# Kernel optimization log

Hardware: AMD Instinct MI355X
Metric: run time of the kernel (lower is better)

## Reference

```python
import jax, jax.numpy as jnp
import numpy as np

Z, Y, X = 16, 128, 128
B = 2
N_R, N_L = 12000, 20000   # active voxels per batch element (radar / lidar)
C = 64
IN_DIM = 4
NUM_LAYER = 2
K_LIST = (64, 32)         # knn fan-out = 64 / 2**layer
EPS = 1e-5


def _make_voxels(rng, n_per_batch):
    # unique voxel coords per batch, sorted by linear index (batch-major rows)
    out = []
    for b in range(B):
        lin = np.sort(rng.choice(Z * Y * X, size=n_per_batch, replace=False))
        z = lin // (Y * X); y = (lin // X) % Y; x = lin % X
        out.append(np.stack([np.full(n_per_batch, b), z, y, x], 1))
    return np.concatenate(out, 0).astype(np.int32)


def _nbr_map(coords):
    # 3x3x3 submanifold-conv rulebook: row index of each neighbor, -1 if absent
    b = coords[:, 0].astype(np.int64); z = coords[:, 1]; y = coords[:, 2]; x = coords[:, 3]
    keys = ((b * Z + z) * Y + y) * X + x  # globally sorted
    N = coords.shape[0]
    nbr = np.full((N, 27), -1, np.int64)
    k = 0
    for dz in (-1, 0, 1):
        for dy in (-1, 0, 1):
            for dx in (-1, 0, 1):
                nz, ny, nx = z + dz, y + dy, x + dx
                ok = (nz >= 0) & (nz < Z) & (ny >= 0) & (ny < Y) & (nx >= 0) & (nx < X)
                cand = ((b * Z + nz) * Y + ny) * X + nx
                pos = np.searchsorted(keys, cand)
                pos_c = np.clip(pos, 0, N - 1)
                hit = ok & (keys[pos_c] == cand)
                nbr[:, k] = np.where(hit, pos_c, -1)
                k += 1
    return nbr


def setup_inputs() -> dict:
    rng = np.random.default_rng(0)
    key = jax.random.key(0)
    ks = jax.random.split(key, 16)
    coordsR = _make_voxels(rng, N_R)
    coordsL = _make_voxels(rng, N_L)
    nbrR = _nbr_map(coordsR)
    nbrL = _nbr_map(coordsL)
    NLt = B * N_L
    # knn indices (global row ids into radar rows of same batch)
    knn0 = coordsL[:, 0:1].astype(np.int64) * N_R + rng.integers(0, N_R, (NLt, K_LIST[0]))
    knn1 = coordsL[:, 0:1].astype(np.int64) * N_R + rng.integers(0, N_R, (NLt, K_LIST[1]))
    sc = 1.0 / np.sqrt(27 * C).astype(np.float32)
    inp = {
        "featR": jax.random.normal(ks[0], (B * N_R, IN_DIM), jnp.float32),
        "featL": jax.random.normal(ks[1], (NLt, IN_DIM), jnp.float32),
        "img": jax.random.normal(ks[2], (B, 512), jnp.float32),
        "Win": jax.random.normal(ks[3], (2, IN_DIM, C), jnp.float32) * 0.1,
        "bin_": jnp.zeros((2, C), jnp.float32),
        # [layer, branch(R/L), conv(sp,subm_a,subm_b), 27, Cin, Cout]
        "Wconv": jax.random.normal(ks[4], (NUM_LAYER, 2, 3, 27, C, C), jnp.float32) * sc,
        "bconv": jnp.zeros((NUM_LAYER, 2, 3, C), jnp.float32),
        "bng": jnp.ones((NUM_LAYER, 2, 3, C), jnp.float32),
        "bnb": jnp.zeros((NUM_LAYER, 2, 3, C), jnp.float32),
        "Wimg": jax.random.normal(ks[5], (NUM_LAYER, 512, C), jnp.float32) * 0.05,
        "bimg": jnp.zeros((NUM_LAYER, C), jnp.float32),
        "Wval": jax.random.normal(ks[6], (NUM_LAYER, C, C), jnp.float32) * 0.125,
        "bval": jnp.zeros((NUM_LAYER, C), jnp.float32),
        "Wgate": jax.random.normal(ks[7], (NUM_LAYER, 2 * C, C), jnp.float32) * 0.09,
        "bgate": jnp.zeros((NUM_LAYER, C), jnp.float32),
        "Wbev": jax.random.normal(ks[8], (NUM_LAYER, 2, C * Z, C, 3, 3), jnp.float32) * (1.0 / np.sqrt(C * Z * 9).astype(np.float32)),
        "bbev": jnp.zeros((NUM_LAYER, 2, C), jnp.float32),
        "bntg": jnp.ones((NUM_LAYER, 2, C), jnp.float32),
        "bntb": jnp.zeros((NUM_LAYER, 2, C), jnp.float32),
        "nbrR": jnp.asarray(nbrR),
        "nbrL": jnp.asarray(nbrL),
        "knn0": jnp.asarray(knn0),
        "knn1": jnp.asarray(knn1),
        "coordsR": jnp.asarray(coordsR),
        "coordsL": jnp.asarray(coordsL),
    }
    return inp


def _bn1d(f, g, b):
    m = f.mean(0)
    v = f.var(0)
    return (f - m) / jnp.sqrt(v + EPS) * g + b


def _sconv(f, nbr, W, bias):
    # gather-scatter sparse 3D conv: out[n] = sum_k W[k] @ f[nbr[n,k]]
    mask = (nbr >= 0)[..., None].astype(f.dtype)
    g = f[jnp.clip(nbr, 0)] * mask                 # [N, 27, C]
    return jnp.einsum('nkc,kcd->nd', g, W) + bias


def _branch_block(f, nbr, Wc, bc, g, bt):
    # spconv -> bn -> relu, subm_a -> bn -> relu, subm_b -> bn -> relu
    for j in range(3):
        f = jax.nn.relu(_bn1d(_sconv(f, nbr, Wc[j], bc[j]), g[j], bt[j]))
    return f


def _to_bev(f, coords, Wt, bt, gg, gb):
    dense = jnp.zeros((B, Z, Y, X, C), f.dtype).at[
        coords[:, 0], coords[:, 1], coords[:, 2], coords[:, 3]].add(f)
    x2 = dense.transpose(0, 4, 1, 2, 3).reshape(B, C * Z, Y, X)  # 'b c z y x -> b (c z) y x'
    # ConvTranspose2d(k=3, s=1, p=1) == conv with swapped-IO, spatially flipped kernel, pad 1
    Wk = jnp.transpose(Wt, (1, 0, 2, 3))[:, :, ::-1, ::-1]
    out = jax.lax.conv_general_dilated(x2, Wk, (1, 1), ((1, 1), (1, 1)),
                                       dimension_numbers=('NCHW', 'OIHW', 'NCHW'))
    out = out + bt[:, None, None]
    m = out.mean((0, 2, 3), keepdims=True)
    v = out.var((0, 2, 3), keepdims=True)
    out = (out - m) / jnp.sqrt(v + EPS) * gg[:, None, None] + gb[:, None, None]
    return jax.nn.relu(out)


def reference(featR, featL, img, Win, bin_, Wconv, bconv, bng, bnb, Wimg, bimg,
              Wval, bval, Wgate, bgate, Wbev, bbev, bntg, bntb,
              nbrR, nbrL, knn0, knn1, coordsR, coordsL):
    fR = featR @ Win[0] + bin_[0]   # input_convR (1x1x1)
    fL = featL @ Win[1] + bin_[1]   # input_convL (1x1x1)
    knns = (knn0, knn1)
    bidL = coordsL[:, 0]
    bevs = []
    for l in range(NUM_LAYER):
        fR = _branch_block(fR, nbrR, Wconv[l, 0], bconv[l, 0], bng[l, 0], bnb[l, 0])
        fL = _branch_block(fL, nbrL, Wconv[l, 1], bconv[l, 1], bng[l, 1], bnb[l, 1])
        # knn cross-attention fusion: lidar queries K nearest radar voxels
        key = fR[knns[l]]                                        # [NL, K, C]
        val = jnp.einsum('nkc,cd->nkd', key, Wval[l]) + bval[l]
        attn = jax.nn.softmax(jnp.einsum('nc,nkc->nk', fL, key), axis=-1)
        fused = jnp.einsum('nk,nkd->nd', attn, val)
        imgf = jax.nn.sigmoid(img @ Wimg[l] + bimg[l])           # [B, C] weather condition
        fused = fused * imgf[bidL]
        gate = jax.nn.sigmoid(jnp.concatenate([fL, fused], -1) @ Wgate[l] + bgate[l])
        fL = fL + gate * fused
        bevs.append(_to_bev(fR, coordsR, Wbev[l, 0], bbev[l, 0], bntg[l, 0], bntb[l, 0]))
        bevs.append(_to_bev(fL, coordsL, Wbev[l, 1], bbev[l, 1], bntg[l, 1], bntb[l, 1]))
    return jnp.concatenate(bevs, axis=1)  # [B, 4*C, Y, X]
```

## Files before the change

kernel.cpp:

```cpp
#include <hip/hip_runtime.h>
#include <math.h>

#define NRT 24000
#define NLT 40000

static __device__ __forceinline__ float sigmoidf_(float x){ return 1.0f/(1.0f+expf(-x)); }

static __device__ __forceinline__ int xcd_swz(int bid, int nwg){
  int q = nwg>>3, r = nwg&7, x = bid&7, i = bid>>3;
  return (x<r ? x*(q+1) : r*(q+1)+(x-r)*q) + i;
}

__global__ void k_proj(const float* __restrict__ feat, const float* __restrict__ W,
                       const float* __restrict__ bias, float* __restrict__ out, int N){
  int i = blockIdx.x*256 + threadIdx.x;
  if (i >= N*64) return;
  int n = i >> 6, c = i & 63;
  const float* f = feat + n*4;
  out[i] = fmaf(f[0], W[c], fmaf(f[1], W[64+c], fmaf(f[2], W[128+c], fmaf(f[3], W[192+c], bias[c]))));
}

__global__ void k_mask(const int* __restrict__ nbr, int N, int* __restrict__ mask){
  int n = blockIdx.x*256+threadIdx.x;
  if (n>=N) return;
  const int* row = nbr + (size_t)n*27;
  int m=0;
  #pragma unroll
  for (int k=0;k<27;k++) if (row[k]>=0) m |= 1<<k;
  mask[n]=m;
}

__global__ void k_wsum(const int* __restrict__ mask, int N, int* __restrict__ wsum){
  int n = blockIdx.x*256+threadIdx.x;
  int pc = (n<N)? __popc(mask[n]) : 0;
  #pragma unroll
  for (int s=32;s;s>>=1) pc += __shfl_down(pc, s, 64);
  if ((threadIdx.x&63)==0) wsum[(blockIdx.x*256+threadIdx.x)>>6] = pc;
}

__global__ void k_scan(const int* __restrict__ in, int M, int* __restrict__ out){
  __shared__ int buf[704];
  for (int i=threadIdx.x;i<M;i+=256) buf[i]=in[i];
  __syncthreads();
  if (threadIdx.x==0){ int s=0; for (int i=0;i<M;i++){ int v=buf[i]; buf[i]=s; s+=v; } buf[M]=s; }
  __syncthreads();
  for (int i=threadIdx.x;i<=M;i+=256) out[i]=buf[i];
}

__global__ void k_noff(const int* __restrict__ mask, const int* __restrict__ woff,
                       int N, int* __restrict__ noff){
  int n = blockIdx.x*256+threadIdx.x;
  if (n>=N) return;
  int lane = threadIdx.x&63;
  int pc = __popc(mask[n]);
  int pre = pc;
  #pragma unroll
  for (int s=1;s<64;s<<=1){ int v=__shfl_up(pre, s, 64); if (lane>=s) pre+=v; }
  noff[n] = woff[n>>6] + pre - pc;
  if (n==N-1) noff[N] = woff[N>>6];
}

__global__ void k_kcnt2(const int* __restrict__ mask, int N, int* __restrict__ cnt2){
  int k = blockIdx.x>>3, seg = blockIdx.x&7;
  int s0 = seg*(N/8), s1 = s0 + N/8;
  int c=0;
  for (int n=s0+threadIdx.x;n<s1;n+=256) c += (mask[n]>>k)&1;
  __shared__ int ls[256];
  ls[threadIdx.x]=c; __syncthreads();
  for (int m=128;m;m>>=1){ if (threadIdx.x<m) ls[threadIdx.x]+=ls[threadIdx.x+m]; __syncthreads(); }
  if (threadIdx.x==0) cnt2[blockIdx.x]=ls[0];
}

__global__ void k_kfill2(const int* __restrict__ mask, int N, const int* __restrict__ off2,
                         unsigned* __restrict__ pairs){
  int w = (blockIdx.x*256+threadIdx.x)>>6;
  int lane = threadIdx.x&63;
  int k = w>>3, seg = w&7;
  int s0 = seg*(N/8), s1 = s0 + N/8;
  int base = off2[w];
  for (int n0=s0;n0<s1;n0+=64){
    int n = n0+lane;
    int v = (n<s1) && ((mask[n]>>k)&1);
    unsigned long long bal = __ballot(v);
    if (v) pairs[base + (int)__popcll(bal & ((1ull<<lane)-1))] = ((unsigned)k<<16)|(unsigned)n;
    base += (int)__popcll(bal);
  }
}

__global__ void k_wc(const float* __restrict__ Wconv, float* __restrict__ WcT){
  int i = blockIdx.x*256+threadIdx.x;
  if (i >= 12*27*16*64*4) return;
  int j = i & 3; int r = i >> 2;
  int d = r & 63; r >>= 6;
  int c4 = r & 15; r >>= 4;
  int k = r % 27; int lc = r / 27;
  WcT[i] = Wconv[(size_t)lc*110592 + (size_t)k*4096 + (size_t)(4*c4+j)*64 + d];
}

__global__ void k_spmm(const float* __restrict__ fin, const int* __restrict__ nbr,
                       const int* __restrict__ mask, const int* __restrict__ noff,
                       const int* __restrict__ off2, const unsigned* __restrict__ pairs,
                       const float* __restrict__ W, float* __restrict__ contrib, int nwaves){
  int wid = (blockIdx.x*256+threadIdx.x)>>6;
  int t = threadIdx.x&63;
  int total = off2[216];
  int a = (int)(((long long)wid*total)/nwaves);
  int b = (int)(((long long)(wid+1)*total)/nwaves);
  int kcur = -1;
  float4 wreg[16];
  for (int i=a;i<b;i++){
    unsigned pk = pairs[i];
    int k = pk>>16, n = pk&0xFFFF;
    if (k!=kcur){
      kcur=k;
      const float4* w4 = reinterpret_cast<const float4*>(W) + k*1024 + t;
      #pragma unroll
      for (int c4=0;c4<16;c4++) wreg[c4]=w4[c4*64];
    }
    int nb = nbr[(size_t)n*27+k];
    const float4* fr = reinterpret_cast<const float4*>(fin + (size_t)nb*64);
    float4 a4 = make_float4(0.f,0.f,0.f,0.f);
    #pragma unroll
    for (int c4=0;c4<16;c4++){
      float4 fv = fr[c4];
      a4.x = fmaf(fv.x, wreg[c4].x, a4.x);
      a4.y = fmaf(fv.y, wreg[c4].y, a4.y);
      a4.z = fmaf(fv.z, wreg[c4].z, a4.z);
      a4.w = fmaf(fv.w, wreg[c4].w, a4.w);
    }
    int rank = __popc(mask[n] & ((1<<k)-1));
    __builtin_nontemporal_store((a4.x+a4.y)+(a4.z+a4.w),
                                &contrib[((size_t)noff[n]+rank)*64 + t]);
  }
}

__global__ void k_sred(const float* __restrict__ contrib, const int* __restrict__ noff,
                       float* __restrict__ out, int N, float* __restrict__ partial){
  int t = threadIdx.x & 63, wv = threadIdx.x >> 6;
  int gw = blockIdx.x*4 + wv;
  float s=0.f, s2=0.f;
  for (int n=gw; n<N; n+=4096){
    int j0=noff[n], j1=noff[n+1];
    float v=0.f;
    for (int j=j0;j<j1;j++) v += __builtin_nontemporal_load(&contrib[(size_t)j*64+t]);
    out[(size_t)n*64+t]=v;
    s += v; s2 = fmaf(v,v,s2);
  }
  __shared__ float ls[4][64], ls2[4][64];
  ls[wv][t]=s; ls2[wv][t]=s2;
  __syncthreads();
  if (wv==0){
    s  = ls[0][t]+ls[1][t]+ls[2][t]+ls[3][t];
    s2 = ls2[0][t]+ls2[1][t]+ls2[2][t]+ls2[3][t];
    partial[(blockIdx.x*64+t)*2+0]=s;
    partial[(blockIdx.x*64+t)*2+1]=s2;
  }
}

__global__ void k_bnfin(const float* __restrict__ partial, int nblk, float invN,
                        const float* __restrict__ g, const float* __restrict__ b,
                        float* __restrict__ mv){
  int t = threadIdx.x, d = t & 63, sub = t >> 6;
  float s=0.f, s2=0.f;
  for (int i=sub;i<nblk;i+=4){ s += partial[(i*64+d)*2]; s2 += partial[(i*64+d)*2+1]; }
  __shared__ float ls[4][64], ls2[4][64];
  ls[sub][d]=s; ls2[sub][d]=s2;
  __syncthreads();
  if (sub==0){
    s  = ls[0][d]+ls[1][d]+ls[2][d]+ls[3][d];
    s2 = ls2[0][d]+ls2[1][d]+ls2[2][d]+ls2[3][d];
    float mean = s*invN;
    float var  = s2*invN - mean*mean;
    float rstd = 1.0f/sqrtf(var + 1e-5f);
    float sc = g[d]*rstd;
    mv[d*2]   = sc;
    mv[d*2+1] = b[d] - mean*sc;
  }
}

__global__ void k_bnrelu(const float* __restrict__ cv, const float* __restrict__ mv,
                         float* __restrict__ fout, int total){
  int i = blockIdx.x*256+threadIdx.x;
  if (i>=total) return;
  int c = i & 63;
  float v = fmaf(cv[i], mv[c*2], mv[c*2+1]);
  fout[i] = v>0.f? v:0.f;
}

__global__ void k_imgf(const float* __restrict__ img, const float* __restrict__ Wimg,
                       const float* __restrict__ bimg, float* __restrict__ imgf){
  int t = threadIdx.x;
  int b = t>>6, c = t&63;
  float s = bimg[c];
  const float* ir = img + b*512;
  for (int j=0;j<512;j++) s = fmaf(ir[j], Wimg[j*64+c], s);
  imgf[b*64+c] = sigmoidf_(s);
}

__global__ void k_attn(float* __restrict__ fL, const float* __restrict__ fR,
                       const int* __restrict__ knn, const int* __restrict__ coordsL,
                       const float* __restrict__ Wval, const float* __restrict__ bval,
                       const float* __restrict__ Wgate, const float* __restrict__ bgate,
                       const float* __restrict__ imgf, int K){
  __shared__ float keys[64*65];
  __shared__ float fls[64];
  __shared__ float aw[64];
  __shared__ float wks[64];
  __shared__ float fus[64];
  int n = blockIdx.x, t = threadIdx.x;
  float fl = fL[(size_t)n*64+t];
  fls[t] = fl;
  const int* kn = knn + (size_t)n*K;
  for (int k=0;k<K;k++){
    int r = kn[k];
    keys[k*65+t] = fR[(size_t)r*64+t];
  }
  __syncthreads();
  float s = -1e30f;
  if (t < K){
    const float* kr = keys + t*65;
    float a0 = 0.f;
    #pragma unroll
    for (int c=0;c<64;c++) a0 = fmaf(fls[c], kr[c], a0);
    s = a0;
  }
  float mx = s;
  #pragma unroll
  for (int m=32;m;m>>=1) mx = fmaxf(mx, __shfl_xor(mx, m, 64));
  float e = (t<K) ? expf(s-mx) : 0.f;
  float se = e;
  #pragma unroll
  for (int m=32;m;m>>=1) se += __shfl_xor(se, m, 64);
  aw[t] = e/se;
  __syncthreads();
  float wk = 0.f;
  for (int k=0;k<K;k++) wk = fmaf(aw[k], keys[k*65+t], wk);
  wks[t] = wk;
  __syncthreads();
  float fu = bval[t];
  #pragma unroll
  for (int c=0;c<64;c++) fu = fmaf(wks[c], Wval[c*64+t], fu);
  int bid = coordsL[n*4];
  fu *= imgf[bid*64+t];
  fus[t] = fu;
  __syncthreads();
  float gs = bgate[t];
  #pragma unroll
  for (int c=0;c<64;c++) gs = fmaf(fls[c], Wgate[c*64+t], gs);
  #pragma unroll
  for (int c=0;c<64;c++) gs = fmaf(fus[c], Wgate[(64+c)*64+t], gs);
  float gate = sigmoidf_(gs);
  fL[(size_t)n*64+t] = fl + gate*fu;
}

__global__ void k_grid(const int* __restrict__ coords, int N, int* __restrict__ grid){
  int n = blockIdx.x*256+threadIdx.x;
  if (n>=N) return;
  int b=coords[n*4], z=coords[n*4+1], y=coords[n*4+2], x=coords[n*4+3];
  grid[((b*128+y)*128+x)*16+z] = n;
}

__global__ void k_colbuild(const int* __restrict__ grid, int* __restrict__ ccnt,
                           int* __restrict__ cent){
  int col = blockIdx.x*256+threadIdx.x;
  if (col >= 2*128*128) return;
  const int* g = grid + col*16;
  int c=0;
  for (int z=0;z<16;z++){ int v=g[z]; if (v>=0) cent[col*16 + (c++)] = (v<<4)|z; }
  ccnt[col]=c;
}

__global__ void k_zbound(const int* __restrict__ coords, int N, int* __restrict__ zs){
  int n = blockIdx.x*256+threadIdx.x;
  if (n>=N) return;
  int key = coords[n*4]*16 + coords[n*4+1];
  int pk = (n>0) ? coords[(n-1)*4]*16 + coords[(n-1)*4+1] : -1;
  for (int kk=pk+1; kk<=key; kk++) zs[kk] = n;
  if (n==N-1){ for (int kk=key+1; kk<=32; kk++) zs[kk] = N; }
}

__global__ void k_wt3(const float* __restrict__ Wbev, float* __restrict__ Wt3){
  int i = blockIdx.x*256+threadIdx.x;
  if (i >= 4*9*16*16*64*4) return;
  int j = i & 3; int r = i >> 2;
  int o = r & 63; r >>= 6;
  int c4 = r & 15; r >>= 4;
  int z = r & 15; r >>= 4;
  int q = r % 9; int ls = r / 9;
  int c = 4*c4 + j;
  int ky = 2-q/3, kx = 2-q%3;
  Wt3[i] = Wbev[(size_t)ls*589824 + (size_t)(c*16+z)*576 + o*9 + ky*3 + kx];
}

__global__ void k_bevg(const float* __restrict__ f, const int* __restrict__ zs,
                       const float* __restrict__ Wt,
                       float* __restrict__ tmp, int CH){
  int blk = xcd_swz(blockIdx.x, gridDim.x);
  int task = blk / CH, chunk = blk % CH;
  int q = task % 9, z = task / 9;
  int t = threadIdx.x & 63, wv = threadIdx.x >> 6;
  const float4* w4 = reinterpret_cast<const float4*>(Wt + (size_t)(((q<<4)+z)<<12)) + t;
  float4 wreg[16];
  #pragma unroll
  for (int c4=0;c4<16;c4++) wreg[c4] = w4[c4*64];
  int s0 = zs[z], c0 = zs[z+1]-s0;
  int s1 = zs[16+z], c1 = zs[17+z]-s1;
  int total = c0 + c1;
  for (int i=chunk*4+wv; i<total; i+=CH*4){
    int v = (i<c0) ? s0+i : s1+(i-c0);
    const float4* fr = reinterpret_cast<const float4*>(f + (size_t)v*64);
    float4 a = make_float4(0.f,0.f,0.f,0.f);
    #pragma unroll
    for (int c4=0;c4<16;c4++){
      float4 fv = fr[c4];
      a.x = fmaf(fv.x, wreg[c4].x, a.x);
      a.y = fmaf(fv.y, wreg[c4].y, a.y);
      a.z = fmaf(fv.z, wreg[c4].z, a.z);
      a.w = fmaf(fv.w, wreg[c4].w, a.w);
    }
    __builtin_nontemporal_store((a.x+a.y)+(a.z+a.w), &tmp[((size_t)v*9+q)*64 + t]);
  }
}

__global__ void k_bevs(const float* __restrict__ tmp, const int* __restrict__ ccnt,
                       const int* __restrict__ cent, float* __restrict__ outp){
  int blk = xcd_swz(blockIdx.x, gridDim.x);
  int b = blk>>12; int rem = blk&4095; int y = rem>>5; int x0 = (rem&31)<<2;
  int t = threadIdx.x;
  float acc[4] = {0.f,0.f,0.f,0.f};
  #pragma unroll
  for (int dy=-1;dy<=1;dy++){
    int y2 = y+dy;
    if ((unsigned)y2 >= 128u) continue;
    int qb = (dy+1)*3 + 1;
    for (int cx=x0-1; cx<=x0+4; cx++){
      if ((unsigned)cx >= 128u) continue;
      int col = ((b<<7)+y2)*128 + cx;
      int cn = ccnt[col];
      const int* ce = cent + col*16;
      int d0 = cx - x0;
      for (int i=0;i<cn;i++){
        int rid = ce[i]>>4;
        const float* tb = tmp + (size_t)rid*576 + qb*64 + t;
        #pragma unroll
        for (int v=0;v<4;v++){
          int dx = d0 - v;
          if (dx>=-1 && dx<=1) acc[v] += __builtin_nontemporal_load(&tb[dx*64]);
        }
      }
    }
  }
  float4 o4 = make_float4(acc[0],acc[1],acc[2],acc[3]);
  *reinterpret_cast<float4*>(outp + (size_t)b*(256*16384) + (size_t)t*16384 + y*128 + x0) = o4;
}

__global__ void k_bevstat(const float* __restrict__ outp, const float* __restrict__ g,
                          const float* __restrict__ b, float* __restrict__ mv){
  int ch = blockIdx.x, t = threadIdx.x;
  float s=0.f, s2=0.f;
  for (int bb=0;bb<2;bb++){
    const float* base = outp + (size_t)bb*(256*16384) + (size_t)ch*16384;
    for (int p=t;p<16384;p+=256){ float v = base[p]; s+=v; s2=fmaf(v,v,s2); }
  }
  __shared__ float ls[256], ls2[256];
  ls[t]=s; ls2[t]=s2; __syncthreads();
  for (int m=128;m;m>>=1){ if (t<m){ ls[t]+=ls[t+m]; ls2[t]+=ls2[t+m]; } __syncthreads(); }
  if (t==0){
    float mean = ls[0]*(1.0f/32768.0f);
    float var  = ls2[0]*(1.0f/32768.0f) - mean*mean;
    float rstd = 1.0f/sqrtf(var+1e-5f);
    float sc = g[ch]*rstd;
    mv[ch*2]=sc; mv[ch*2+1]=b[ch]-mean*sc;
  }
}

__global__ void k_bevbn(float* __restrict__ outp, const float* __restrict__ mv){
  int i = blockIdx.x*256+threadIdx.x;
  if (i >= 2*64*16384) return;
  int bb = i>>20; int r = i & ((1<<20)-1);
  int ch = r>>14; int p = r&16383;
  float* a = outp + (size_t)bb*(256*16384) + (size_t)ch*16384 + p;
  float v = fmaf(*a, mv[ch*2], mv[ch*2+1]);
  *a = v>0.f? v:0.f;
}

extern "C" void kernel_launch(void* const* d_in, const int* in_sizes, int n_in,
                              void* d_out, int out_size, void* d_ws, size_t ws_size,
                              hipStream_t stream){
  const float* featR = (const float*)d_in[0];
  const float* featL = (const float*)d_in[1];
  const float* img   = (const float*)d_in[2];
  const float* Win   = (const float*)d_in[3];
  const float* bin_  = (const float*)d_in[4];
  const float* Wconv = (const float*)d_in[5];
  const float* bng   = (const float*)d_in[7];
  const float* bnb   = (const float*)d_in[8];
  const float* Wimg  = (const float*)d_in[9];
  const float* bimg  = (const float*)d_in[10];
  const float* Wval  = (const float*)d_in[11];
  const float* bval  = (const float*)d_in[12];
  const float* Wgate = (const float*)d_in[13];
  const float* bgate = (const float*)d_in[14];
  const float* Wbev  = (const float*)d_in[15];
  const float* bntg  = (const float*)d_in[17];
  const float* bntb  = (const float*)d_in[18];
  const int* nbrR    = (const int*)d_in[19];
  const int* nbrL    = (const int*)d_in[20];
  const int* knn0    = (const int*)d_in[21];
  const int* knn1    = (const int*)d_in[22];
  const int* coordsR = (const int*)d_in[23];
  const int* coordsL = (const int*)d_in[24];
  float* outp = (float*)d_out;

  char* w = (char*)d_ws;
  auto alloc = [&](size_t bytes){ char* p = w; w += (bytes + 255) & ~(size_t)255; return p; };
  float* fRa = (float*)alloc((size_t)NRT*64*4);
  float* fLa = (float*)alloc((size_t)NLT*64*4);
  int*   gridR = (int*)alloc((size_t)2*128*128*16*4);
  int*   gridL = (int*)alloc((size_t)2*128*128*16*4);
  float* Wt3 = (float*)alloc((size_t)4*9*16*16*64*4*4);
  float* WcT = (float*)alloc((size_t)12*27*16*64*4*4);
  float* imgfbuf = (float*)alloc(2*64*4);
  float* partial = (float*)alloc((size_t)1024*64*2*4);
  float* mv = (float*)alloc(64*2*4);
  int* ccntR = (int*)alloc((size_t)2*128*128*4);
  int* ccntL = (int*)alloc((size_t)2*128*128*4);
  int* centR = (int*)alloc((size_t)2*128*128*16*4);
  int* centL = (int*)alloc((size_t)2*128*128*16*4);
  int* zsR = (int*)alloc(33*4);
  int* zsL = (int*)alloc(33*4);
  int* maskR = (int*)alloc((size_t)NRT*4);
  int* maskL = (int*)alloc((size_t)NLT*4);
  int* wsumR = (int*)alloc(1024*4);
  int* wsumL = (int*)alloc(1024*4);
  int* woffR = (int*)alloc(1024*4);
  int* woffL = (int*)alloc(1024*4);
  int* noffR = (int*)alloc((size_t)(NRT+1)*4);
  int* noffL = (int*)alloc((size_t)(NLT+1)*4);
  int* cnt2R = (int*)alloc(256*4);
  int* cnt2L = (int*)alloc(256*4);
  int* off2R = (int*)alloc(256*4);
  int* off2L = (int*)alloc(256*4);
  unsigned* pairsR = (unsigned*)alloc((size_t)6*NRT*4);
  unsigned* pairsL = (unsigned*)alloc((size_t)6*NLT*4);
  char* big = alloc((size_t)NLT*576*4);
  float* cv      = (float*)big;
  float* contrib = (float*)(big + (size_t)16*1024*1024);
  float* tmp     = (float*)big;

  hipMemsetAsync(gridR, 0xFF, (size_t)2*128*128*16*4, stream);
  hipMemsetAsync(gridL, 0xFF, (size_t)2*128*128*16*4, stream);
  k_grid<<<(NRT+255)/256,256,0,stream>>>(coordsR, NRT, gridR);
  k_grid<<<(NLT+255)/256,256,0,stream>>>(coordsL, NLT, gridL);
  k_colbuild<<<(2*128*128+255)/256,256,0,stream>>>(gridR, ccntR, centR);
  k_colbuild<<<(2*128*128+255)/256,256,0,stream>>>(gridL, ccntL, centL);
  k_zbound<<<(NRT+255)/256,256,0,stream>>>(coordsR, NRT, zsR);
  k_zbound<<<(NLT+255)/256,256,0,stream>>>(coordsL, NLT, zsL);
  k_mask<<<(NRT+255)/256,256,0,stream>>>(nbrR, NRT, maskR);
  k_mask<<<(NLT+255)/256,256,0,stream>>>(nbrL, NLT, maskL);
  k_wsum<<<(NRT+255)/256,256,0,stream>>>(maskR, NRT, wsumR);
  k_wsum<<<(NLT+255)/256,256,0,stream>>>(maskL, NLT, wsumL);
  k_scan<<<1,256,0,stream>>>(wsumR, NRT/64, woffR);
  k_scan<<<1,256,0,stream>>>(wsumL, NLT/64, woffL);
  k_noff<<<(NRT+255)/256,256,0,stream>>>(maskR, woffR, NRT, noffR);
  k_noff<<<(NLT+255)/256,256,0,stream>>>(maskL, woffL, NLT, noffL);
  k_kcnt2<<<216,256,0,stream>>>(maskR, NRT, cnt2R);
  k_kcnt2<<<216,256,0,stream>>>(maskL, NLT, cnt2L);
  k_scan<<<1,256,0,stream>>>(cnt2R, 216, off2R);
  k_scan<<<1,256,0,stream>>>(cnt2L, 216, off2L);
  k_kfill2<<<54,256,0,stream>>>(maskR, NRT, off2R, pairsR);
  k_kfill2<<<54,256,0,stream>>>(maskL, NLT, off2L, pairsL);
  k_wt3<<<(4*9*16*16*64*4+255)/256,256,0,stream>>>(Wbev, Wt3);
  k_wc<<<(12*27*16*64*4+255)/256,256,0,stream>>>(Wconv, WcT);

  k_proj<<<(NRT*64+255)/256,256,0,stream>>>(featR, Win,     bin_,    fRa, NRT);
  k_proj<<<(NLT*64+255)/256,256,0,stream>>>(featL, Win+256, bin_+64, fLa, NLT);

  const int CH = 8;
  const int NWV = 8192;
  for (int l=0;l<2;l++){
    for (int j=0;j<3;j++){
      const float* Wc = WcT + (size_t)((l*2+0)*3+j)*110592;
      k_spmm<<<NWV/4,256,0,stream>>>(fRa, nbrR, maskR, noffR, off2R, pairsR, Wc, contrib, NWV);
      k_sred<<<1024,256,0,stream>>>(contrib, noffR, cv, NRT, partial);
      k_bnfin<<<1,256,0,stream>>>(partial, 1024, 1.0f/NRT,
                                  bng + ((l*2+0)*3+j)*64, bnb + ((l*2+0)*3+j)*64, mv);
      k_bnrelu<<<(NRT*64+255)/256,256,0,stream>>>(cv, mv, fRa, NRT*64);
    }
    for (int j=0;j<3;j++){
      const float* Wc = WcT + (size_t)((l*2+1)*3+j)*110592;
      k_spmm<<<NWV/4,256,0,stream>>>(fLa, nbrL, maskL, noffL, off2L, pairsL, Wc, contrib, NWV);
      k_sred<<<1024,256,0,stream>>>(contrib, noffL, cv, NLT, partial);
      k_bnfin<<<1,256,0,stream>>>(partial, 1024, 1.0f/NLT,
                                  bng + ((l*2+1)*3+j)*64, bnb + ((l*2+1)*3+j)*64, mv);
      k_bnrelu<<<(NLT*64+255)/256,256,0,stream>>>(cv, mv, fLa, NLT*64);
    }
    k_imgf<<<1,128,0,stream>>>(img, Wimg + (size_t)l*512*64, bimg + l*64, imgfbuf);
    const int* knn = (l==0)? knn0 : knn1;
    int K = (l==0)? 64 : 32;
    k_attn<<<NLT,64,0,stream>>>(fLa, fRa, knn, coordsL,
                                Wval + (size_t)l*4096, bval + l*64,
                                Wgate + (size_t)l*8192, bgate + l*64,
                                imgfbuf, K);
    {
      float* op = outp + (size_t)(2*l)*64*16384;
      const float* wt = Wt3 + (size_t)(l*2+0)*589824;
      k_bevg<<<144*CH,256,0,stream>>>(fRa, zsR, wt, tmp, CH);
      k_bevs<<<2*128*32,64,0,stream>>>(tmp, ccntR, centR, op);
      k_bevstat<<<64,256,0,stream>>>(op, bntg + (l*2+0)*64, bntb + (l*2+0)*64, mv);
      k_bevbn<<<(2*64*16384+255)/256,256,0,stream>>>(op, mv);
    }
    {
      float* op = outp + (size_t)(2*l+1)*64*16384;
      const float* wt = Wt3 + (size_t)(l*2+1)*589824;
      k_bevg<<<144*CH,256,0,stream>>>(fLa, zsL, wt, tmp, CH);
      k_bevs<<<2*128*32,64,0,stream>>>(tmp, ccntL, centL, op);
      k_bevstat<<<64,256,0,stream>>>(op, bntg + (l*2+1)*64, bntb + (l*2+1)*64, mv);
      k_bevbn<<<(2*64*16384+255)/256,256,0,stream>>>(op, mv);
    }
  }
}
```

Before: 3.299 ms.

## Vectorize BN kernels, split BEV tmp into per-tap planes, unroll bevg by two

Several changes at once. The BN+ReLU, BEV stat and BEV BN kernels now use float4 loads and stores. The BEV temporary buffer changes from a voxel-major [v][9][64] layout to per-tap planes [q][v][64]. k_bevg processes two voxels per iteration and runs with CH doubled. Together these aim to cut instruction count and improve store and load coalescing in the elementwise and BEV stages, at the cost of more register pressure in k_bevg and less locality in k_bevs, which now reads across tap planes.

```diff
diff --git a/kernel.cpp b/kernel.cpp
--- a/kernel.cpp
+++ b/kernel.cpp
@@ -178,13 +178,17 @@
   }
 }
 
-__global__ void k_bnrelu(const float* __restrict__ cv, const float* __restrict__ mv,
-                         float* __restrict__ fout, int total){
+__global__ void k_bnrelu(const float4* __restrict__ cv, const float* __restrict__ mv,
+                         float4* __restrict__ fout, int total4){
   int i = blockIdx.x*256+threadIdx.x;
-  if (i>=total) return;
-  int c = i & 63;
-  float v = fmaf(cv[i], mv[c*2], mv[c*2+1]);
-  fout[i] = v>0.f? v:0.f;
+  if (i>=total4) return;
+  int c = (i & 15)*4;
+  float4 v = cv[i];
+  v.x = fmaf(v.x, mv[(c+0)*2], mv[(c+0)*2+1]); v.x = v.x>0.f? v.x:0.f;
+  v.y = fmaf(v.y, mv[(c+1)*2], mv[(c+1)*2+1]); v.y = v.y>0.f? v.y:0.f;
+  v.z = fmaf(v.z, mv[(c+2)*2], mv[(c+2)*2+1]); v.z = v.z>0.f? v.z:0.f;
+  v.w = fmaf(v.w, mv[(c+3)*2], mv[(c+3)*2+1]); v.w = v.w>0.f? v.w:0.f;
+  fout[i] = v;
 }
 
 __global__ void k_imgf(const float* __restrict__ img, const float* __restrict__ Wimg,
@@ -294,7 +298,7 @@
 
 __global__ void k_bevg(const float* __restrict__ f, const int* __restrict__ zs,
                        const float* __restrict__ Wt,
-                       float* __restrict__ tmp, int CH){
+                       float* __restrict__ tmp, int CH, size_t PL){
   int blk = xcd_swz(blockIdx.x, gridDim.x);
   int task = blk / CH, chunk = blk % CH;
   int q = task % 9, z = task / 9;
@@ -306,24 +310,38 @@
   int s0 = zs[z], c0 = zs[z+1]-s0;
   int s1 = zs[16+z], c1 = zs[17+z]-s1;
   int total = c0 + c1;
-  for (int i=chunk*4+wv; i<total; i+=CH*4){
-    int v = (i<c0) ? s0+i : s1+(i-c0);
-    const float4* fr = reinterpret_cast<const float4*>(f + (size_t)v*64);
+  float* tq = tmp + (size_t)q*PL;
+  int stride = CH*4;
+  for (int i=chunk*4+wv; i<total; i+=2*stride){
+    int i2 = i + stride;
+    bool has2 = i2 < total;
+    int v  = (i <c0) ? s0+i  : s1+(i -c0);
+    int v2 = has2 ? ((i2<c0) ? s0+i2 : s1+(i2-c0)) : v;
+    const float4* fr  = reinterpret_cast<const float4*>(f + (size_t)v *64);
+    const float4* fr2 = reinterpret_cast<const float4*>(f + (size_t)v2*64);
     float4 a = make_float4(0.f,0.f,0.f,0.f);
+    float4 b = make_float4(0.f,0.f,0.f,0.f);
     #pragma unroll
     for (int c4=0;c4<16;c4++){
-      float4 fv = fr[c4];
-      a.x = fmaf(fv.x, wreg[c4].x, a.x);
-      a.y = fmaf(fv.y, wreg[c4].y, a.y);
-      a.z = fmaf(fv.z, wreg[c4].z, a.z);
-      a.w = fmaf(fv.w, wreg[c4].w, a.w);
-    }
-    __builtin_nontemporal_store((a.x+a.y)+(a.z+a.w), &tmp[((size_t)v*9+q)*64 + t]);
+      float4 fv  = fr[c4];
+      float4 fv2 = fr2[c4];
+      a.x = fmaf(fv.x,  wreg[c4].x, a.x);
+      a.y = fmaf(fv.y,  wreg[c4].y, a.y);
+      a.z = fmaf(fv.z,  wreg[c4].z, a.z);
+      a.w = fmaf(fv.w,  wreg[c4].w, a.w);
+      b.x = fmaf(fv2.x, wreg[c4].x, b.x);
+      b.y = fmaf(fv2.y, wreg[c4].y, b.y);
+      b.z = fmaf(fv2.z, wreg[c4].z, b.z);
+      b.w = fmaf(fv2.w, wreg[c4].w, b.w);
+    }
+    __builtin_nontemporal_store((a.x+a.y)+(a.z+a.w), &tq[(size_t)v*64 + t]);
+    if (has2)
+      __builtin_nontemporal_store((b.x+b.y)+(b.z+b.w), &tq[(size_t)v2*64 + t]);
   }
 }
 
 __global__ void k_bevs(const float* __restrict__ tmp, const int* __restrict__ ccnt,
-                       const int* __restrict__ cent, float* __restrict__ outp){
+                       const int* __restrict__ cent, float* __restrict__ outp, size_t PL){
   int blk = xcd_swz(blockIdx.x, gridDim.x);
   int b = blk>>12; int rem = blk&4095; int y = rem>>5; int x0 = (rem&31)<<2;
   int t = threadIdx.x;
@@ -341,11 +359,12 @@
       int d0 = cx - x0;
       for (int i=0;i<cn;i++){
         int rid = ce[i]>>4;
-        const float* tb = tmp + (size_t)rid*576 + qb*64 + t;
+        const float* tb = tmp + (size_t)qb*PL + (size_t)rid*64 + t;
         #pragma unroll
         for (int v=0;v<4;v++){
           int dx = d0 - v;
-          if (dx>=-1 && dx<=1) acc[v] += __builtin_nontemporal_load(&tb[dx*64]);
+          if (dx>=-1 && dx<=1)
+            acc[v] += __builtin_nontemporal_load(tb + (ptrdiff_t)dx*(ptrdiff_t)PL);
         }
       }
     }
@@ -359,8 +378,13 @@
   int ch = blockIdx.x, t = threadIdx.x;
   float s=0.f, s2=0.f;
   for (int bb=0;bb<2;bb++){
-    const float* base = outp + (size_t)bb*(256*16384) + (size_t)ch*16384;
-    for (int p=t;p<16384;p+=256){ float v = base[p]; s+=v; s2=fmaf(v,v,s2); }
+    const float4* base = reinterpret_cast<const float4*>(outp + (size_t)bb*(256*16384) + (size_t)ch*16384);
+    for (int p=t;p<4096;p+=256){
+      float4 v = base[p];
+      s += (v.x+v.y)+(v.z+v.w);
+      s2 = fmaf(v.x,v.x,s2); s2 = fmaf(v.y,v.y,s2);
+      s2 = fmaf(v.z,v.z,s2); s2 = fmaf(v.w,v.w,s2);
+    }
   }
   __shared__ float ls[256], ls2[256];
   ls[t]=s; ls2[t]=s2; __syncthreads();
@@ -374,14 +398,20 @@
   }
 }
 
-__global__ void k_bevbn(float* __restrict__ outp, const float* __restrict__ mv){
+__global__ void k_bevbn(float* __restrict__ op, const float* __restrict__ mv){
   int i = blockIdx.x*256+threadIdx.x;
-  if (i >= 2*64*16384) return;
-  int bb = i>>20; int r = i & ((1<<20)-1);
-  int ch = r>>14; int p = r&16383;
-  float* a = outp + (size_t)bb*(256*16384) + (size_t)ch*16384 + p;
-  float v = fmaf(*a, mv[ch*2], mv[ch*2+1]);
-  *a = v>0.f? v:0.f;
+  if (i >= 2*64*4096) return;
+  int bb = i >> 18;
+  int ch = (i >> 12) & 63;
+  int p  = i & 4095;
+  float4* a = reinterpret_cast<float4*>(op) + (size_t)bb*(256*4096) + (size_t)ch*4096 + p;
+  float sc = mv[ch*2], sh = mv[ch*2+1];
+  float4 v = *a;
+  v.x = fmaf(v.x, sc, sh); v.x = v.x>0.f? v.x:0.f;
+  v.y = fmaf(v.y, sc, sh); v.y = v.y>0.f? v.y:0.f;
+  v.z = fmaf(v.z, sc, sh); v.z = v.z>0.f? v.z:0.f;
+  v.w = fmaf(v.w, sc, sh); v.w = v.w>0.f? v.w:0.f;
+  *a = v;
 }
 
 extern "C" void kernel_launch(void* const* d_in, const int* in_sizes, int n_in,
@@ -476,8 +506,9 @@
   k_proj<<<(NRT*64+255)/256,256,0,stream>>>(featR, Win,     bin_,    fRa, NRT);
   k_proj<<<(NLT*64+255)/256,256,0,stream>>>(featL, Win+256, bin_+64, fLa, NLT);
 
-  const int CH = 8;
+  const int CH = 16;
   const int NWV = 8192;
+  const size_t PLR = (size_t)NRT*64, PLL = (size_t)NLT*64;
   for (int l=0;l<2;l++){
     for (int j=0;j<3;j++){
       const float* Wc = WcT + (size_t)((l*2+0)*3+j)*110592;
@@ -485,7 +516,7 @@
       k_sred<<<1024,256,0,stream>>>(contrib, noffR, cv, NRT, partial);
       k_bnfin<<<1,256,0,stream>>>(partial, 1024, 1.0f/NRT,
                                   bng + ((l*2+0)*3+j)*64, bnb + ((l*2+0)*3+j)*64, mv);
-      k_bnrelu<<<(NRT*64+255)/256,256,0,stream>>>(cv, mv, fRa, NRT*64);
+      k_bnrelu<<<(NRT*16+255)/256,256,0,stream>>>((const float4*)cv, mv, (float4*)fRa, NRT*16);
     }
     for (int j=0;j<3;j++){
       const float* Wc = WcT + (size_t)((l*2+1)*3+j)*110592;
@@ -493,7 +524,7 @@
       k_sred<<<1024,256,0,stream>>>(contrib, noffL, cv, NLT, partial);
       k_bnfin<<<1,256,0,stream>>>(partial, 1024, 1.0f/NLT,
                                   bng + ((l*2+1)*3+j)*64, bnb + ((l*2+1)*3+j)*64, mv);
-      k_bnrelu<<<(NLT*64+255)/256,256,0,stream>>>(cv, mv, fLa, NLT*64);
+      k_bnrelu<<<(NLT*16+255)/256,256,0,stream>>>((const float4*)cv, mv, (float4*)fLa, NLT*16);
     }
     k_imgf<<<1,128,0,stream>>>(img, Wimg + (size_t)l*512*64, bimg + l*64, imgfbuf);
     const int* knn = (l==0)? knn0 : knn1;
@@ -505,18 +536,18 @@
     {
       float* op = outp + (size_t)(2*l)*64*16384;
       const float* wt = Wt3 + (size_t)(l*2+0)*589824;
-      k_bevg<<<144*CH,256,0,stream>>>(fRa, zsR, wt, tmp, CH);
-      k_bevs<<<2*128*32,64,0,stream>>>(tmp, ccntR, centR, op);
+      k_bevg<<<144*CH,256,0,stream>>>(fRa, zsR, wt, tmp, CH, PLR);
+      k_bevs<<<2*128*32,64,0,stream>>>(tmp, ccntR, centR, op, PLR);
       k_bevstat<<<64,256,0,stream>>>(op, bntg + (l*2+0)*64, bntb + (l*2+0)*64, mv);
-      k_bevbn<<<(2*64*16384+255)/256,256,0,stream>>>(op, mv);
+      k_bevbn<<<(2*64*4096+255)/256,256,0,stream>>>(op, mv);
     }
     {
       float* op = outp + (size_t)(2*l+1)*64*16384;
       const float* wt = Wt3 + (size_t)(l*2+1)*589824;
-      k_bevg<<<144*CH,256,0,stream>>>(fLa, zsL, wt, tmp, CH);
-      k_bevs<<<2*128*32,64,0,stream>>>(tmp, ccntL, centL, op);
+      k_bevg<<<144*CH,256,0,stream>>>(fLa, zsL, wt, tmp, CH, PLL);
+      k_bevs<<<2*128*32,64,0,stream>>>(tmp, ccntL, centL, op, PLL);
       k_bevstat<<<64,256,0,stream>>>(op, bntg + (l*2+1)*64, bntb + (l*2+1)*64, mv);
-      k_bevbn<<<(2*64*16384+255)/256,256,0,stream>>>(op, mv);
-    }
-  }
-}
+      k_bevbn<<<(2*64*4096+255)/256,256,0,stream>>>(op, mv);
+    }
+  }
+}
```

After: 3.904 ms. 1.18x slower.
